# Kernel optimization log

Hardware: AMD Instinct MI355X
Metric: run time of the kernel (lower is better)

Reference implementation:

```python
import jax, jax.numpy as jnp
import numpy as np

N_HEAD = 8


def _norm(x):
    # torch: (x - x.mean()) / x.std()  -- global, unbiased std (ddof=1)
    return (x - x.mean()) / x.std(ddof=1)


def _floyd_block2(x, w_qkv, scale):
    # x: [b, n, n, c]; w_qkv: [5c, c] (torch Linear weight layout)
    x = _norm(x)
    b, n, _, c = x.shape
    qkv = x @ w_qkv.T  # [b, n, n, 5c]
    q, k1, k2, v1, v2 = jnp.split(qkv, 5, axis=-1)

    def heads(t):  # 'b i j (h d) -> b h i j d'
        return t.reshape(b, n, n, N_HEAD, c // N_HEAD).transpose(0, 3, 1, 2, 4)

    q, k1, k2, v1, v2 = map(heads, (q, k1, k2, v1, v2))
    # pivotal attention: for pair (i,j) attend over pivot p with two k/v branches
    s = (jnp.einsum('bhijd,bhipd->bhijp', q, k1)
         + jnp.einsum('bhijd,bhpjd->bhijp', q, k2)) * scale  # [b,h,i,j,p]
    a = jax.nn.softmax(s, axis=-1)
    o = (jnp.einsum('bhijp,bhipd->bhijd', a, v1)
         + jnp.einsum('bhijp,bhpjd->bhijd', a, v2))
    # 'b h i j d -> b i j (h d)'
    return o.transpose(0, 2, 3, 1, 4).reshape(b, n, n, c)


def setup_inputs() -> dict:
    key = jax.random.key(0)
    k1, k2, k3, k4 = jax.random.split(key, 4)
    b, n, c, depth = 4, 96, 256, 4
    adj = jax.random.randint(k1, (b, n, n), 0, 2, dtype=jnp.int64)
    emb_w = jax.random.normal(k2, (128, c), dtype=jnp.float32)  # std 1.0 per init_weights
    qkv_w = jax.random.normal(k3, (depth, 5 * c, c), dtype=jnp.float32) * (c ** -0.5)
    head_w = jax.random.normal(k4, (c, c), dtype=jnp.float32) * 0.02
    head_b = jnp.zeros((c,), dtype=jnp.float32)
    return {'adj': adj, 'emb_w': emb_w, 'qkv_w': qkv_w,
            'head_w': head_w, 'head_b': head_b}


def reference(adj, emb_w, qkv_w, head_w, head_b):
    c = emb_w.shape[1]
    head_dim = c // N_HEAD
    scale = head_dim ** (-0.5) * 50.0  # FloydBlock2 scale
    x = emb_w[adj]  # [b, n, n, c]
    for l in range(qkv_w.shape[0]):
        x = _floyd_block2(x, qkv_w[l], scale)
    x = x.mean(axis=(1, 2))           # mean over (i, j) -> [b, c]
    x = jax.lax.stop_gradient(x)      # blocks run under torch.no_grad
    return x @ head_w.T + head_b
```

## Files before the change

kernel.cpp:

```cpp
#include <hip/hip_runtime.h>

#define B_ 4
#define N_ 96
#define C_ 256
#define NPAIR (B_*N_*N_)
#define CE (NPAIR*C_)
#define SCALE 8.838834764831844f
#define CP 132

typedef __attribute__((ext_vector_type(4))) float f32x4;
typedef __attribute__((ext_vector_type(8))) __bf16 bf16x8;
typedef __attribute__((ext_vector_type(4))) __bf16 bf16x4;
typedef __attribute__((ext_vector_type(4))) unsigned short u16x4;
typedef __attribute__((ext_vector_type(8))) unsigned short u16x8;

__device__ __forceinline__ unsigned short f2bf(float f){
  __bf16 h = (__bf16)f;
  return __builtin_bit_cast(unsigned short, h);
}
__device__ __forceinline__ float bf2f(unsigned short u){
  union { unsigned int i; float f; } v; v.i = ((unsigned int)u) << 16; return v.f;
}
__device__ __forceinline__ f32x4 vmax4(f32x4 a, f32x4 b){
  f32x4 r; r.x=fmaxf(a.x,b.x); r.y=fmaxf(a.y,b.y); r.z=fmaxf(a.z,b.z); r.w=fmaxf(a.w,b.w); return r;
}

__device__ __forceinline__ void gload16(const void* g, void* l){
  __builtin_amdgcn_global_load_lds((const __attribute__((address_space(1))) unsigned int*)g,
                                   (__attribute__((address_space(3))) unsigned int*)l,
                                   16, 0, 0);
}

__global__ __launch_bounds__(256) void k_init(float* __restrict__ z){
  for (int i = threadIdx.x; i < 1536; i += 256) z[i] = 0.f;
}

__global__ __launch_bounds__(256) void k_gather(const int* __restrict__ adj,
                                                const float* __restrict__ emb,
                                                unsigned short* __restrict__ xb,
                                                float2* __restrict__ part){
  int tid = threadIdx.x;
  int lp = tid >> 4, lane16 = tid & 15;
  int pair = blockIdx.x*16 + lp;
  int row = adj[pair];
  const f32x4* src = (const f32x4*)(emb + (size_t)row*C_);
  u16x4*       dst = (u16x4*)(xb + (size_t)pair*C_);
  float s = 0.f, q = 0.f;
  for (int v = 0; v < 4; ++v){
    f32x4 t = src[v*16 + lane16];
    u16x4 o;
    o.x = f2bf(t.x); o.y = f2bf(t.y); o.z = f2bf(t.z); o.w = f2bf(t.w);
    dst[v*16 + lane16] = o;
    s += t.x + t.y + t.z + t.w;
    q += t.x*t.x + t.y*t.y + t.z*t.z + t.w*t.w;
  }
  __shared__ float rs[256], rq[256];
  rs[tid] = s; rq[tid] = q; __syncthreads();
  for (int o = 128; o > 0; o >>= 1){
    if (tid < o){ rs[tid] += rs[tid+o]; rq[tid] += rq[tid+o]; }
    __syncthreads();
  }
  if (tid == 0){
    float* pp = (float*)&part[blockIdx.x & 63];
    atomicAdd(pp, rs[0]); atomicAdd(pp+1, rq[0]);
  }
}

__global__ __launch_bounds__(256) void k_wconv(const float* __restrict__ w,
                                               unsigned short* __restrict__ wb,
                                               float* __restrict__ wsum){
  int row  = blockIdx.x*4 + (threadIdx.x >> 6);
  int lane = threadIdx.x & 63;
  f32x4 v = ((const f32x4*)(w + (size_t)row*256))[lane];
  u16x4 o;
  o.x = f2bf(v.x); o.y = f2bf(v.y); o.z = f2bf(v.z); o.w = f2bf(v.w);
  ((u16x4*)(wb + (size_t)row*256))[lane] = o;
  float s = v.x + v.y + v.z + v.w;
  for (int m = 32; m > 0; m >>= 1) s += __shfl_down(s, m);
  if (lane == 0) wsum[row] = s;
}

__global__ __launch_bounds__(256) void k_gemm(const unsigned short* __restrict__ Xb,
                                              const unsigned short* __restrict__ W,
                                              const float* __restrict__ wsum_l,
                                              const float2* __restrict__ part,
                                              unsigned short* __restrict__ qkv5){
  __shared__ unsigned short smem[128*CP];
  unsigned short* As = smem;
  unsigned short* Bs = smem + 128*64;
  const int tid = threadIdx.x;
  const int w = tid >> 6, lane = tid & 63;
  const int quad = lane >> 4, l16 = lane & 15;
  const int L = blockIdx.x;
  const int xcd = L & 7, rest = L >> 3;
  const int nt = rest % 10, kt2 = rest / 10;
  const int m0 = (xcd + 8*kt2) * 128, n0 = nt * 128;
  const int mw = (w & 1) * 64, nw = (w >> 1) * 64;
  double S = 0.0, Q = 0.0;
  for (int i = 0; i < 64; ++i){ float2 pp = part[i]; S += (double)pp.x; Q += (double)pp.y; }
  const float mean = (float)(S / (double)CE);
  const float rstd = (float)(1.0 / sqrt((Q - S*S/(double)CE) / (double)(CE - 1)));
  f32x4 acc[4][4] = {};

  for (int kt = 0; kt < 256; kt += 64){
    const int rbase = w * 32;
    const int rowoff = lane >> 3;
    const int kg = (lane & 7) ^ rowoff;
    for (int i8 = 0; i8 < 4; ++i8){
      int row = rbase + i8*8 + rowoff;
      gload16(Xb + (size_t)(m0+row)*256 + kt + kg*8, &As[(rbase + i8*8)*64]);
      gload16(W  + (size_t)(n0+row)*256 + kt + kg*8, &Bs[(rbase + i8*8)*64]);
    }
    __syncthreads();
    for (int ks = 0; ks < 2; ++ks){
      bf16x8 af[4], bf[4];
      for (int t4 = 0; t4 < 4; ++t4){
        int rm = mw + t4*16 + l16;
        af[t4] = *(const bf16x8*)((const char*)As + rm*128 + ((((ks<<2)|quad) ^ (rm&7))*16));
        int rn = nw + t4*16 + l16;
        bf[t4] = *(const bf16x8*)((const char*)Bs + rn*128 + ((((ks<<2)|quad) ^ (rn&7))*16));
      }
      for (int mi = 0; mi < 4; ++mi)
        for (int ni = 0; ni < 4; ++ni)
          acc[mi][ni] = __builtin_amdgcn_mfma_f32_16x16x32_bf16(af[mi], bf[ni], acc[mi][ni], 0, 0, 0);
    }
    __syncthreads();
  }

  float ws[4];
  #pragma unroll
  for (int ni = 0; ni < 4; ++ni) ws[ni] = wsum_l[n0 + nw + ni*16 + l16];
  for (int mi = 0; mi < 4; ++mi)
    for (int ni = 0; ni < 4; ++ni)
      for (int r = 0; r < 4; ++r){
        int row = mw + mi*16 + quad*4 + r;
        int col = nw + ni*16 + l16;
        float val = rstd*(acc[mi][ni][r] - mean*ws[ni]);
        smem[row*CP + col] = f2bf(val);
      }
  __syncthreads();

  const int t_slab = n0 >> 8;
  const int hbase  = (n0 >> 5) & 7;
  unsigned short* slab = qkv5 + (size_t)t_slab*CE;
  const int trow = tid >> 4;
  const int tcol = (tid & 15) * 8;
  const int h  = hbase + (tcol >> 5);
  const int dd = tcol & 31;
  for (int pass = 0; pass < 8; ++pass){
    int row = pass*16 + trow;
    int gm = m0 + row;
    int b = gm / 9216; int rem = gm - b*9216;
    int ii = rem / 96, jj = rem - (rem/96)*96;
    u16x8 vv = *(const u16x8*)&smem[row*CP + tcol];
    *(u16x8*)&slab[(((size_t)(b*8+h)*96 + ii)*96 + jj)*32 + dd] = vv;
  }
}

__global__ __launch_bounds__(256) void k_scores1(const unsigned short* __restrict__ qkv5,
                                                 unsigned short* __restrict__ s1){
  __shared__ unsigned short Qs[96*40], Ks[96*40];
  __shared__ unsigned short Ss[96*100];
  int wg = blockIdx.x; int bh = wg/96, ic = wg - bh*96;
  int tid = threadIdx.x;
  size_t gslab = (size_t)wg*3072;
  const unsigned short* qp = qkv5 + 0*(size_t)CE + gslab;
  const unsigned short* kp = qkv5 + 1*(size_t)CE + gslab;
  for (int g = tid; g < 768; g += 256){
    int j = g >> 3, q4 = g & 7;
    *(u16x4*)&Qs[j*40 + q4*4] = *(const u16x4*)&qp[j*32 + q4*4];
    *(u16x4*)&Ks[j*40 + q4*4] = *(const u16x4*)&kp[j*32 + q4*4];
  }
  __syncthreads();
  int w = tid >> 6, lane = tid & 63, quad = lane >> 4, l16 = lane & 15;
  #pragma unroll
  for (int r = 0; r < 9; ++r){
    int tile = w*9 + r; int jt = tile/6, pt = tile - jt*6;
    bf16x8 a = *(const bf16x8*)((const char*)Qs + (jt*16 + l16)*80 + quad*16);
    bf16x8 b = *(const bf16x8*)((const char*)Ks + (pt*16 + l16)*80 + quad*16);
    f32x4 cc = {0.f,0.f,0.f,0.f};
    cc = __builtin_amdgcn_mfma_f32_16x16x32_bf16(a, b, cc, 0, 0, 0);
    int col = pt*16 + l16;
    #pragma unroll
    for (int rr = 0; rr < 4; ++rr){
      int row = jt*16 + quad*4 + rr;
      _Float16 hv = (_Float16)(cc[rr] * SCALE);
      Ss[row*100 + col] = __builtin_bit_cast(unsigned short, hv);
    }
  }
  __syncthreads();
  for (int g = tid; g < 1152; g += 256){
    int j = g / 12, c8 = g - j*12;
    *(u16x8*)&s1[((size_t)(bh*96 + j))*9216 + ic*96 + c8*8] = *(const u16x8*)&Ss[j*100 + c8*8];
  }
}

__global__ __launch_bounds__(256) void k_attn2(const unsigned short* __restrict__ qkv5,
                                               const unsigned short* __restrict__ s1,
                                               unsigned short* __restrict__ a_out,
                                               unsigned short* __restrict__ xb,
                                               float* __restrict__ poolAcc,
                                               int last){
  __shared__ unsigned short Qs[96*40];
  __shared__ unsigned short Ks[96*40];
  __shared__ unsigned short SsPb[96*104];
  __shared__ float Mx[192], Sx[192];
  __shared__ float poolL[32];
  unsigned short* Vd = Qs;
  const int L = blockIdx.x;
  const int virt = (L & 7)*384 + (L >> 3);
  int bh = virt/96, jj = virt - bh*96;
  int b = bh >> 3, h = bh & 7;
  int tid = threadIdx.x;
  int w = tid >> 6, lane = tid & 63, quad = lane >> 4, l16 = lane & 15;
  const unsigned short* qn  = qkv5 + 0*(size_t)CE;
  const unsigned short* k2n = qkv5 + 2*(size_t)CE;
  const unsigned short* v2n = qkv5 + 4*(size_t)CE;
  if (tid < 192){ Mx[tid] = -1e30f; Sx[tid] = 0.f; }
  if (tid < 32) poolL[tid] = 0.f;
  const unsigned short* s1g = s1 + ((size_t)bh*96 + jj)*9216;
  for (int g = tid; g < 1152; g += 256){
    int i = g / 12, c8 = g - i*12;
    *(u16x8*)&SsPb[i*100 + c8*8] = *(const u16x8*)&s1g[i*96 + c8*8];
  }
  for (int g = tid; g < 768; g += 256){
    int r7 = g & 7, q4 = (g >> 3) & 7, a8 = g >> 6;
    int p = r7 + a8*8;
    size_t base = (((size_t)bh*96 + p)*96 + jj)*32 + q4*4;
    *(u16x4*)&Qs[p*40 + q4*4] = *(const u16x4*)&qn[base];
    *(u16x4*)&Ks[p*40 + q4*4] = *(const u16x4*)&k2n[base];
  }
  __syncthreads();
  f32x4 sc[9];
  #pragma unroll
  for (int r = 0; r < 9; ++r){
    int tile = w*9 + r; int it = tile/6, pt = tile - it*6;
    bf16x8 a = *(const bf16x8*)((const char*)Qs + (it*16 + l16)*80 + quad*16);
    bf16x8 bb = *(const bf16x8*)((const char*)Ks + (pt*16 + l16)*80 + quad*16);
    f32x4 cc = {0.f,0.f,0.f,0.f};
    cc = __builtin_amdgcn_mfma_f32_16x16x32_bf16(a, bb, cc, 0, 0, 0);
    int col = pt*16 + l16;
    #pragma unroll
    for (int rr = 0; rr < 4; ++rr){
      int row = it*16 + quad*4 + rr;
      _Float16 hv = __builtin_bit_cast(_Float16, SsPb[row*100 + col]);
      sc[r][rr] = cc[rr]*SCALE + (float)hv;
    }
  }
  const bool odd = (w & 1);
  const int itA = (w*9)/6, itB = itA + 1;
  const int slot = w & 1;
  f32x4 vA = {-1e30f,-1e30f,-1e30f,-1e30f}, vB = vA;
  #pragma unroll
  for (int r = 0; r < 9; ++r){
    bool inA = odd ? (r < 3) : (r < 6);
    if (inA) vA = vmax4(vA, sc[r]); else vB = vmax4(vB, sc[r]);
  }
  #pragma unroll
  for (int m = 1; m < 16; m <<= 1){
    f32x4 t;
    t.x=__shfl_xor(vA.x,m); t.y=__shfl_xor(vA.y,m); t.z=__shfl_xor(vA.z,m); t.w=__shfl_xor(vA.w,m);
    vA = vmax4(vA, t);
    t.x=__shfl_xor(vB.x,m); t.y=__shfl_xor(vB.y,m); t.z=__shfl_xor(vB.z,m); t.w=__shfl_xor(vB.w,m);
    vB = vmax4(vB, t);
  }
  if (l16 < 4){
    float va = (l16==0)?vA.x:(l16==1)?vA.y:(l16==2)?vA.z:vA.w;
    float vb = (l16==0)?vB.x:(l16==1)?vB.y:(l16==2)?vB.z:vB.w;
    Mx[(itA*16 + quad*4 + l16)*2 + slot] = va;
    Mx[(itB*16 + quad*4 + l16)*2 + slot] = vb;
  }
  __syncthreads();
  for (int g = tid; g < 768; g += 256){
    int r7 = g & 7, q4 = (g >> 3) & 7, a8 = g >> 6;
    int p = r7 + a8*8;
    u16x4 v = *(const u16x4*)&v2n[(((size_t)bh*96 + p)*96 + jj)*32 + q4*4];
    int d0 = q4*4;
    Vd[(d0+0)*100 + p] = v.x; Vd[(d0+1)*100 + p] = v.y;
    Vd[(d0+2)*100 + p] = v.z; Vd[(d0+3)*100 + p] = v.w;
  }
  f32x4 mA, mB;
  #pragma unroll
  for (int rr = 0; rr < 4; ++rr){
    float2 ta = *(const float2*)&Mx[(itA*16 + quad*4 + rr)*2];
    float2 tb = *(const float2*)&Mx[(itB*16 + quad*4 + rr)*2];
    mA[rr] = fmaxf(ta.x, ta.y); mB[rr] = fmaxf(tb.x, tb.y);
  }
  f32x4 sA = {0.f,0.f,0.f,0.f}, sB = {0.f,0.f,0.f,0.f};
  #pragma unroll
  for (int r = 0; r < 9; ++r){
    bool inA = odd ? (r < 3) : (r < 6);
    #pragma unroll
    for (int rr = 0; rr < 4; ++rr){
      float m = inA ? mA[rr] : mB[rr];
      float e = __expf(sc[r][rr] - m);
      sc[r][rr] = e;
      if (inA) sA[rr] += e; else sB[rr] += e;
    }
  }
  #pragma unroll
  for (int m = 1; m < 16; m <<= 1){
    f32x4 t;
    t.x=__shfl_xor(sA.x,m); t.y=__shfl_xor(sA.y,m); t.z=__shfl_xor(sA.z,m); t.w=__shfl_xor(sA.w,m);
    sA += t;
    t.x=__shfl_xor(sB.x,m); t.y=__shfl_xor(sB.y,m); t.z=__shfl_xor(sB.z,m); t.w=__shfl_xor(sB.w,m);
    sB += t;
  }
  if (l16 < 4){
    float va = (l16==0)?sA.x:(l16==1)?sA.y:(l16==2)?sA.z:sA.w;
    float vb = (l16==0)?sB.x:(l16==1)?sB.y:(l16==2)?sB.z:sB.w;
    Sx[(itA*16 + quad*4 + l16)*2 + slot] = va;
    Sx[(itB*16 + quad*4 + l16)*2 + slot] = vb;
  }
  __syncthreads();
  f32x4 iA, iB;
  #pragma unroll
  for (int rr = 0; rr < 4; ++rr){
    float2 ta = *(const float2*)&Sx[(itA*16 + quad*4 + rr)*2];
    float2 tb = *(const float2*)&Sx[(itB*16 + quad*4 + rr)*2];
    iA[rr] = 1.f/(ta.x + ta.y); iB[rr] = 1.f/(tb.x + tb.y);
  }
  #pragma unroll
  for (int r = 0; r < 9; ++r){
    int tile = w*9 + r; int it = tile/6, pt = tile - it*6;
    int col = pt*16 + l16;
    bool inA = odd ? (r < 3) : (r < 6);
    #pragma unroll
    for (int rr = 0; rr < 4; ++rr){
      int row = it*16 + quad*4 + rr;
      float inv = inA ? iA[rr] : iB[rr];
      SsPb[row*104 + col] = f2bf(sc[r][rr] * inv);
    }
  }
  __syncthreads();
  unsigned short* ap = a_out + (size_t)bh*96*9216 + (size_t)jj*96;
  for (int g = tid; g < 1152; g += 256){
    int i = g / 12, cc = g - i*12;
    *(u16x8*)&ap[(size_t)i*9216 + cc*8] = *(const u16x8*)&SsPb[i*104 + cc*8];
  }
  #pragma unroll
  for (int r = 0; r < 3; ++r){
    int tile = w*3 + r; int it = tile >> 1, dt = tile & 1;
    f32x4 cc = {0.f,0.f,0.f,0.f};
    #pragma unroll
    for (int kp3 = 0; kp3 < 3; ++kp3){
      bf16x8 a = *(const bf16x8*)((const char*)SsPb + (it*16 + l16)*208 + kp3*64 + quad*16);
      const char* vb = (const char*)Vd + (dt*16 + l16)*200 + kp3*64 + quad*16;
      bf16x4 lo = *(const bf16x4*)vb;
      bf16x4 hi = *(const bf16x4*)(vb + 8);
      bf16x8 bb = __builtin_shufflevector(lo, hi, 0,1,2,3,4,5,6,7);
      cc = __builtin_amdgcn_mfma_f32_16x16x32_bf16(a, bb, cc, 0, 0, 0);
    }
    int d = dt*16 + l16;
    if (!last){
      #pragma unroll
      for (int rr = 0; rr < 4; ++rr){
        int i = it*16 + quad*4 + rr;
        xb[(((size_t)b*96 + i)*96 + jj)*256 + h*32 + d] = f2bf(cc[rr]);
      }
    } else {
      atomicAdd(&poolL[d], cc[0] + cc[1] + cc[2] + cc[3]);
    }
  }
  if (last){
    __syncthreads();
    if (tid < 32) atomicAdd(&poolAcc[b*256 + h*32 + tid], poolL[tid]);
  }
}

__global__ __launch_bounds__(256) void k_attn1(const unsigned short* __restrict__ a_in,
                                               const unsigned short* __restrict__ qkv5,
                                               unsigned short* __restrict__ xb,
                                               float2* __restrict__ statsPart,
                                               float* __restrict__ poolAcc,
                                               int last){
  __shared__ unsigned short As[96*104], Vd[32*100];
  __shared__ float redS[256], redQ[256];
  __shared__ float poolL[32];
  int wg = blockIdx.x; int bh = wg/96, ii = wg - bh*96;
  int b = bh >> 3, h = bh & 7;
  int tid = threadIdx.x;
  if (tid < 32) poolL[tid] = 0.f;
  const unsigned short* vp = qkv5 + 3*(size_t)CE + ((size_t)bh*96 + ii)*3072;
  for (int g = tid; g < 768; g += 256){
    int r7 = g & 7, q4 = (g >> 3) & 7, a8 = g >> 6;
    int p = r7 + a8*8;
    u16x4 v = *(const u16x4*)&vp[p*32 + q4*4];
    int d0 = q4*4;
    Vd[(d0+0)*100 + p] = v.x; Vd[(d0+1)*100 + p] = v.y;
    Vd[(d0+2)*100 + p] = v.z; Vd[(d0+3)*100 + p] = v.w;
  }
  const unsigned short* ain = a_in + ((size_t)bh*96 + ii)*9216;
  for (int g = tid; g < 1152; g += 256){
    int j = g / 12, cc = g - j*12;
    *(u16x8*)&As[j*104 + cc*8] = *(const u16x8*)&ain[j*96 + cc*8];
  }
  __syncthreads();
  int w = tid >> 6, lane = tid & 63, quad = lane >> 4, l16 = lane & 15;
  float ls = 0.f, lq = 0.f;
  #pragma unroll
  for (int r = 0; r < 3; ++r){
    int tile = w*3 + r; int jt = tile >> 1, dt = tile & 1;
    f32x4 cc = {0.f,0.f,0.f,0.f};
    #pragma unroll
    for (int kp3 = 0; kp3 < 3; ++kp3){
      bf16x8 a = *(const bf16x8*)((const char*)As + (jt*16 + l16)*208 + kp3*64 + quad*16);
      const char* vb = (const char*)Vd + (dt*16 + l16)*200 + kp3*64 + quad*16;
      bf16x4 lo = *(const bf16x4*)vb;
      bf16x4 hi = *(const bf16x4*)(vb + 8);
      bf16x8 bb = __builtin_shufflevector(lo, hi, 0,1,2,3,4,5,6,7);
      cc = __builtin_amdgcn_mfma_f32_16x16x32_bf16(a, bb, cc, 0, 0, 0);
    }
    int d = dt*16 + l16;
    if (!last){
      #pragma unroll
      for (int rr = 0; rr < 4; ++rr){
        int j = jt*16 + quad*4 + rr;
        size_t xi = (((size_t)b*96 + ii)*96 + j)*256 + h*32 + d;
        float val = bf2f(xb[xi]) + cc[rr];
        xb[xi] = f2bf(val); ls += val; lq += val*val;
      }
    } else {
      atomicAdd(&poolL[d], cc[0] + cc[1] + cc[2] + cc[3]);
    }
  }
  if (!last){
    redS[tid] = ls; redQ[tid] = lq; __syncthreads();
    for (int o = 128; o > 0; o >>= 1){
      if (tid < o){ redS[tid] += redS[tid+o]; redQ[tid] += redQ[tid+o]; }
      __syncthreads();
    }
    if (tid == 0){
      float* pp = (float*)&statsPart[blockIdx.x & 63];
      atomicAdd(pp, redS[0]); atomicAdd(pp+1, redQ[0]);
    }
  } else {
    __syncthreads();
    if (tid < 32) atomicAdd(&poolAcc[b*256 + h*32 + tid], poolL[tid]);
  }
}

__global__ __launch_bounds__(256) void k_head(const float* __restrict__ poolAcc,
                                              const float* __restrict__ hw,
                                              const float* __restrict__ hb,
                                              float* __restrict__ out){
  int b = blockIdx.x, t = threadIdx.x;
  __shared__ float xm[256];
  xm[t] = poolAcc[b*256 + t] * (1.0f/9216.0f);
  __syncthreads();
  float o = hb[t];
  for (int cc = 0; cc < 256; ++cc) o += xm[cc] * hw[t*256 + cc];
  out[b*256 + t] = o;
}

extern "C" void kernel_launch(void* const* d_in, const int* in_sizes, int n_in,
                              void* d_out, int out_size, void* d_ws, size_t ws_size,
                              hipStream_t stream){
  (void)in_sizes; (void)n_in; (void)out_size; (void)ws_size;
  const int*   adj  = (const int*)d_in[0];
  const float* emb  = (const float*)d_in[1];
  const float* qkvw = (const float*)d_in[2];
  const float* hw   = (const float*)d_in[3];
  const float* hb   = (const float*)d_in[4];

  char* p = (char*)d_ws;
  unsigned short* xb   = (unsigned short*)p; p += (size_t)CE*2;
  unsigned short* qkv5 = (unsigned short*)p; p += (size_t)5*CE*2;
  unsigned short* s1   = (unsigned short*)p; p += (size_t)32*96*9216*2;
  unsigned short* aP   = (unsigned short*)p; p += (size_t)32*96*9216*2;
  unsigned short* wbf  = (unsigned short*)p; p += (size_t)4*1280*256*2;
  float*          wsum = (float*)p;          p += (size_t)4*1280*4;
  float2*         part = (float2*)p;         p += 4*64*sizeof(float2);
  float*          pool = (float*)p;          p += 1024*sizeof(float);

  k_init  <<<dim3(1),     dim3(256), 0, stream>>>((float*)part);
  k_gather<<<dim3(2304),  dim3(256), 0, stream>>>(adj, emb, xb, part);
  k_wconv <<<dim3(1280),  dim3(256), 0, stream>>>(qkvw, wbf, wsum);
  for (int l = 0; l < 4; ++l){
    int last = (l == 3) ? 1 : 0;
    k_gemm   <<<dim3(2880),    dim3(256), 0, stream>>>(xb, wbf + (size_t)l*1280*256,
                                                       wsum + l*1280, part + l*64, qkv5);
    k_scores1<<<dim3(3072),    dim3(256), 0, stream>>>(qkv5, s1);
    k_attn2  <<<dim3(3072),    dim3(256), 0, stream>>>(qkv5, s1, aP, xb, pool, last);
    k_attn1  <<<dim3(3072),    dim3(256), 0, stream>>>(aP, qkv5, xb,
                                                       part + (l+1 < 4 ? (l+1)*64 : 0),
                                                       pool, last);
  }
  k_head<<<dim3(4), dim3(256), 0, stream>>>(pool, hw, hb, (float*)d_out);
}
```

Before: 620.2 us.

## Cut LDS use in attention kernels: direct score stores, aliased buffers, shuffle reductions

k_scores1 now writes fp16 scores straight from MFMA registers to global memory instead of staging them in shared memory, dropping a barrier and an LDS buffer. k_attn2 aliases Q/K and the probability tile into one shared buffer and reads the s1 bias directly from global memory. Loads move to 16-byte vectors, and k_attn1's tree reduction becomes wavefront shuffles. The aim is less LDS footprint for higher occupancy and fewer barriers, at the cost of scattered 2-byte global stores and uncoalesced global reads of s1.

```diff
diff --git a/kernel.cpp b/kernel.cpp
--- a/kernel.cpp
+++ b/kernel.cpp
@@ -160,19 +160,19 @@
 __global__ __launch_bounds__(256) void k_scores1(const unsigned short* __restrict__ qkv5,
                                                  unsigned short* __restrict__ s1){
   __shared__ unsigned short Qs[96*40], Ks[96*40];
-  __shared__ unsigned short Ss[96*100];
   int wg = blockIdx.x; int bh = wg/96, ic = wg - bh*96;
   int tid = threadIdx.x;
   size_t gslab = (size_t)wg*3072;
   const unsigned short* qp = qkv5 + 0*(size_t)CE + gslab;
   const unsigned short* kp = qkv5 + 1*(size_t)CE + gslab;
-  for (int g = tid; g < 768; g += 256){
-    int j = g >> 3, q4 = g & 7;
-    *(u16x4*)&Qs[j*40 + q4*4] = *(const u16x4*)&qp[j*32 + q4*4];
-    *(u16x4*)&Ks[j*40 + q4*4] = *(const u16x4*)&kp[j*32 + q4*4];
+  for (int g = tid; g < 384; g += 256){
+    int j = g >> 2, d8 = (g & 3)*8;
+    *(u16x8*)&Qs[j*40 + d8] = *(const u16x8*)&qp[j*32 + d8];
+    *(u16x8*)&Ks[j*40 + d8] = *(const u16x8*)&kp[j*32 + d8];
   }
   __syncthreads();
   int w = tid >> 6, lane = tid & 63, quad = lane >> 4, l16 = lane & 15;
+  unsigned short* s1o = s1 + (size_t)bh*96*9216;
   #pragma unroll
   for (int r = 0; r < 9; ++r){
     int tile = w*9 + r; int jt = tile/6, pt = tile - jt*6;
@@ -185,13 +185,8 @@
     for (int rr = 0; rr < 4; ++rr){
       int row = jt*16 + quad*4 + rr;
       _Float16 hv = (_Float16)(cc[rr] * SCALE);
-      Ss[row*100 + col] = __builtin_bit_cast(unsigned short, hv);
-    }
-  }
-  __syncthreads();
-  for (int g = tid; g < 1152; g += 256){
-    int j = g / 12, c8 = g - j*12;
-    *(u16x8*)&s1[((size_t)(bh*96 + j))*9216 + ic*96 + c8*8] = *(const u16x8*)&Ss[j*100 + c8*8];
+      s1o[(size_t)row*9216 + ic*96 + col] = __builtin_bit_cast(unsigned short, hv);
+    }
   }
 }
 
@@ -201,12 +196,10 @@
                                                unsigned short* __restrict__ xb,
                                                float* __restrict__ poolAcc,
                                                int last){
-  __shared__ unsigned short Qs[96*40];
-  __shared__ unsigned short Ks[96*40];
-  __shared__ unsigned short SsPb[96*104];
+  __shared__ unsigned short Sh[96*100];
+  __shared__ unsigned short VdM[32*100];
   __shared__ float Mx[192], Sx[192];
-  __shared__ float poolL[32];
-  unsigned short* Vd = Qs;
+  float* poolL = Mx;
   const int L = blockIdx.x;
   const int virt = (L & 7)*384 + (L >> 3);
   int bh = virt/96, jj = virt - bh*96;
@@ -217,33 +210,27 @@
   const unsigned short* k2n = qkv5 + 2*(size_t)CE;
   const unsigned short* v2n = qkv5 + 4*(size_t)CE;
   if (tid < 192){ Mx[tid] = -1e30f; Sx[tid] = 0.f; }
-  if (tid < 32) poolL[tid] = 0.f;
+  for (int g = tid; g < 384; g += 256){
+    int d8 = (g & 3)*8, p = g >> 2;
+    size_t base = (((size_t)bh*96 + p)*96 + jj)*32 + d8;
+    *(u16x8*)&Sh[p*40 + d8]        = *(const u16x8*)&qn[base];
+    *(u16x8*)&Sh[3840 + p*40 + d8] = *(const u16x8*)&k2n[base];
+  }
+  __syncthreads();
   const unsigned short* s1g = s1 + ((size_t)bh*96 + jj)*9216;
-  for (int g = tid; g < 1152; g += 256){
-    int i = g / 12, c8 = g - i*12;
-    *(u16x8*)&SsPb[i*100 + c8*8] = *(const u16x8*)&s1g[i*96 + c8*8];
-  }
-  for (int g = tid; g < 768; g += 256){
-    int r7 = g & 7, q4 = (g >> 3) & 7, a8 = g >> 6;
-    int p = r7 + a8*8;
-    size_t base = (((size_t)bh*96 + p)*96 + jj)*32 + q4*4;
-    *(u16x4*)&Qs[p*40 + q4*4] = *(const u16x4*)&qn[base];
-    *(u16x4*)&Ks[p*40 + q4*4] = *(const u16x4*)&k2n[base];
-  }
-  __syncthreads();
   f32x4 sc[9];
   #pragma unroll
   for (int r = 0; r < 9; ++r){
     int tile = w*9 + r; int it = tile/6, pt = tile - it*6;
-    bf16x8 a = *(const bf16x8*)((const char*)Qs + (it*16 + l16)*80 + quad*16);
-    bf16x8 bb = *(const bf16x8*)((const char*)Ks + (pt*16 + l16)*80 + quad*16);
+    bf16x8 a  = *(const bf16x8*)((const char*)Sh + (it*16 + l16)*80 + quad*16);
+    bf16x8 bb = *(const bf16x8*)((const char*)Sh + 7680 + (pt*16 + l16)*80 + quad*16);
     f32x4 cc = {0.f,0.f,0.f,0.f};
     cc = __builtin_amdgcn_mfma_f32_16x16x32_bf16(a, bb, cc, 0, 0, 0);
     int col = pt*16 + l16;
     #pragma unroll
     for (int rr = 0; rr < 4; ++rr){
       int row = it*16 + quad*4 + rr;
-      _Float16 hv = __builtin_bit_cast(_Float16, SsPb[row*100 + col]);
+      _Float16 hv = __builtin_bit_cast(_Float16, s1g[(size_t)row*96 + col]);
       sc[r][rr] = cc[rr]*SCALE + (float)hv;
     }
   }
@@ -271,13 +258,11 @@
     Mx[(itB*16 + quad*4 + l16)*2 + slot] = vb;
   }
   __syncthreads();
-  for (int g = tid; g < 768; g += 256){
-    int r7 = g & 7, q4 = (g >> 3) & 7, a8 = g >> 6;
-    int p = r7 + a8*8;
-    u16x4 v = *(const u16x4*)&v2n[(((size_t)bh*96 + p)*96 + jj)*32 + q4*4];
-    int d0 = q4*4;
-    Vd[(d0+0)*100 + p] = v.x; Vd[(d0+1)*100 + p] = v.y;
-    Vd[(d0+2)*100 + p] = v.z; Vd[(d0+3)*100 + p] = v.w;
+  for (int g = tid; g < 384; g += 256){
+    int d8 = (g & 3)*8, p = g >> 2;
+    u16x8 v = *(const u16x8*)&v2n[(((size_t)bh*96 + p)*96 + jj)*32 + d8];
+    #pragma unroll
+    for (int k = 0; k < 8; ++k) VdM[(d8+k)*100 + p] = v[k];
   }
   f32x4 mA, mB;
   #pragma unroll
@@ -313,6 +298,7 @@
     Sx[(itB*16 + quad*4 + l16)*2 + slot] = vb;
   }
   __syncthreads();
+  if (last && tid < 32) poolL[tid] = 0.f;
   f32x4 iA, iB;
   #pragma unroll
   for (int rr = 0; rr < 4; ++rr){
@@ -329,14 +315,14 @@
     for (int rr = 0; rr < 4; ++rr){
       int row = it*16 + quad*4 + rr;
       float inv = inA ? iA[rr] : iB[rr];
-      SsPb[row*104 + col] = f2bf(sc[r][rr] * inv);
+      Sh[row*100 + col] = f2bf(sc[r][rr] * inv);
     }
   }
   __syncthreads();
   unsigned short* ap = a_out + (size_t)bh*96*9216 + (size_t)jj*96;
-  for (int g = tid; g < 1152; g += 256){
-    int i = g / 12, cc = g - i*12;
-    *(u16x8*)&ap[(size_t)i*9216 + cc*8] = *(const u16x8*)&SsPb[i*104 + cc*8];
+  for (int g = tid; g < 2304; g += 256){
+    int i = g / 24, c4 = g - i*24;
+    *(u16x4*)&ap[(size_t)i*9216 + c4*4] = *(const u16x4*)&Sh[i*100 + c4*4];
   }
   #pragma unroll
   for (int r = 0; r < 3; ++r){
@@ -344,12 +330,15 @@
     f32x4 cc = {0.f,0.f,0.f,0.f};
     #pragma unroll
     for (int kp3 = 0; kp3 < 3; ++kp3){
-      bf16x8 a = *(const bf16x8*)((const char*)SsPb + (it*16 + l16)*208 + kp3*64 + quad*16);
-      const char* vb = (const char*)Vd + (dt*16 + l16)*200 + kp3*64 + quad*16;
+      const char* pa = (const char*)Sh + (it*16 + l16)*200 + kp3*64 + quad*16;
+      bf16x4 alo = *(const bf16x4*)pa;
+      bf16x4 ahi = *(const bf16x4*)(pa + 8);
+      bf16x8 a = __builtin_shufflevector(alo, ahi, 0,1,2,3,4,5,6,7);
+      const char* vb = (const char*)VdM + (dt*16 + l16)*200 + kp3*64 + quad*16;
       bf16x4 lo = *(const bf16x4*)vb;
       bf16x4 hi = *(const bf16x4*)(vb + 8);
-      bf16x8 bb = __builtin_shufflevector(lo, hi, 0,1,2,3,4,5,6,7);
-      cc = __builtin_amdgcn_mfma_f32_16x16x32_bf16(a, bb, cc, 0, 0, 0);
+      bf16x8 bbv = __builtin_shufflevector(lo, hi, 0,1,2,3,4,5,6,7);
+      cc = __builtin_amdgcn_mfma_f32_16x16x32_bf16(a, bbv, cc, 0, 0, 0);
     }
     int d = dt*16 + l16;
     if (!last){
@@ -375,20 +364,18 @@
                                                float* __restrict__ poolAcc,
                                                int last){
   __shared__ unsigned short As[96*104], Vd[32*100];
-  __shared__ float redS[256], redQ[256];
+  __shared__ float redW[8];
   __shared__ float poolL[32];
   int wg = blockIdx.x; int bh = wg/96, ii = wg - bh*96;
   int b = bh >> 3, h = bh & 7;
   int tid = threadIdx.x;
   if (tid < 32) poolL[tid] = 0.f;
   const unsigned short* vp = qkv5 + 3*(size_t)CE + ((size_t)bh*96 + ii)*3072;
-  for (int g = tid; g < 768; g += 256){
-    int r7 = g & 7, q4 = (g >> 3) & 7, a8 = g >> 6;
-    int p = r7 + a8*8;
-    u16x4 v = *(const u16x4*)&vp[p*32 + q4*4];
-    int d0 = q4*4;
-    Vd[(d0+0)*100 + p] = v.x; Vd[(d0+1)*100 + p] = v.y;
-    Vd[(d0+2)*100 + p] = v.z; Vd[(d0+3)*100 + p] = v.w;
+  for (int g = tid; g < 384; g += 256){
+    int d8 = (g & 3)*8, p = g >> 2;
+    u16x8 v = *(const u16x8*)&vp[p*32 + d8];
+    #pragma unroll
+    for (int k = 0; k < 8; ++k) Vd[(d8+k)*100 + p] = v[k];
   }
   const unsigned short* ain = a_in + ((size_t)bh*96 + ii)*9216;
   for (int g = tid; g < 1152; g += 256){
@@ -425,14 +412,15 @@
     }
   }
   if (!last){
-    redS[tid] = ls; redQ[tid] = lq; __syncthreads();
-    for (int o = 128; o > 0; o >>= 1){
-      if (tid < o){ redS[tid] += redS[tid+o]; redQ[tid] += redQ[tid+o]; }
-      __syncthreads();
-    }
+    #pragma unroll
+    for (int m = 32; m > 0; m >>= 1){ ls += __shfl_down(ls, m); lq += __shfl_down(lq, m); }
+    if (lane == 0){ redW[w] = ls; redW[4+w] = lq; }
+    __syncthreads();
     if (tid == 0){
+      float S = redW[0]+redW[1]+redW[2]+redW[3];
+      float Q = redW[4]+redW[5]+redW[6]+redW[7];
       float* pp = (float*)&statsPart[blockIdx.x & 63];
-      atomicAdd(pp, redS[0]); atomicAdd(pp+1, redQ[0]);
+      atomicAdd(pp, S); atomicAdd(pp+1, Q);
     }
   } else {
     __syncthreads();
```

New measurement: 595.0 us. 4.1% less time.
